# Kernel tuning notes

Measured on AMD Instinct MI355X. Metric: run time of the kernel, lower is better.

Reference implementation:

```python
import jax, jax.numpy as jnp
import numpy as np

N_NODES = 28


def _gcn_norm(edge_index, n):
    """PyG GCNConv normalization: add self-loops, sym-normalize by deg^-1/2."""
    loops = jnp.arange(n, dtype=edge_index.dtype)
    src = jnp.concatenate([edge_index[0], loops])
    dst = jnp.concatenate([edge_index[1], loops])
    ones = jnp.ones(src.shape[0], dtype=jnp.float32)
    deg = jax.ops.segment_sum(ones, dst, num_segments=n)  # in-degree incl. self-loop
    dinv = jnp.where(deg > 0, 1.0 / jnp.sqrt(deg), 0.0)
    norm = dinv[src] * dinv[dst]  # [E+N]
    return src, dst, norm


def _gcn_conv(x, W, b, src, dst, norm, n):
    # x: [B, N, Cin] -> [B, N, Cout]; linear first, then normalized scatter-add.
    h = jnp.einsum('bni,io->bno', x, W)
    msg = h[:, src, :] * norm[None, :, None]          # gather + edge scaling
    out = jnp.zeros_like(h).at[:, dst, :].add(msg)     # scatter-add over dst
    return out + b


def setup_inputs() -> dict:
    key = jax.random.key(0)
    k1, k2, k3, k4 = jax.random.split(key, 4)
    B, N, E, H = 65536, N_NODES, 756, 64
    x = jax.random.normal(k1, (B, N), dtype=jnp.float32)
    edge_index = jax.random.randint(k2, (2, E), 0, N, dtype=jnp.int64)
    W1 = jax.random.normal(k3, (1, H), dtype=jnp.float32) * (1.0 / np.sqrt(1.0))
    b1 = jnp.zeros((H,), dtype=jnp.float32)
    W2 = jax.random.normal(k4, (H, 1), dtype=jnp.float32) * (1.0 / np.sqrt(H))
    b2 = jnp.zeros((1,), dtype=jnp.float32)
    return {"x": x, "edge_index": edge_index, "W1": W1, "b1": b1, "W2": W2, "b2": b2}


def reference(x, edge_index, W1, b1, W2, b2):
    n = x.shape[1]
    src, dst, norm = _gcn_norm(edge_index, n)
    h = x[:, :, None]                                  # [B, N, 1] node features
    h = jax.nn.relu(_gcn_conv(h, W1, b1, src, dst, norm, n))
    # dropout(0.2) is identity in eval mode
    h = _gcn_conv(h, W2, b2, src, dst, norm, n)        # [B, N, 1]
    return h[:, :, 0]
```

## Files before the change

### kernel.cpp

```cpp
#include <hip/hip_runtime.h>
#include <math.h>

#define NN 28
#define NH 64

__global__ __launch_bounds__(256) void build_graph_kernel(
    const int* __restrict__ ei, int E,
    const float* __restrict__ W1, const float* __restrict__ b1,
    const float* __restrict__ W2, float* __restrict__ ws) {
  __shared__ float dinv[NN];
  __shared__ float A[NN * NN];
  __shared__ float cpos, cneg;
  __shared__ int flag;
  const int t = threadIdx.x;

  if (t < NN) dinv[t] = 1.0f;
  for (int i = t; i < NN * NN; i += blockDim.x) A[i] = 0.0f;
  if (t == 0) { cpos = 0.0f; cneg = 0.0f; flag = 0; }
  __syncthreads();

  for (int e = t; e < E; e += blockDim.x) {
    int d = ei[E + e];
    atomicAdd(&dinv[d], 1.0f);
  }
  __syncthreads();
  if (t < NN) dinv[t] = 1.0f / sqrtf(dinv[t]);
  __syncthreads();

  for (int e = t; e < E; e += blockDim.x) {
    int s = ei[e];
    int d = ei[E + e];
    atomicAdd(&A[d * NN + s], dinv[s] * dinv[d]);
  }
  if (t < NN) atomicAdd(&A[t * NN + t], dinv[t] * dinv[t]);

  if (t < NH) {
    float w1 = W1[t], w2 = W2[t];
    if (w1 > 0.0f)      atomicAdd(&cpos, w1 * w2);
    else if (w1 < 0.0f) atomicAdd(&cneg, w1 * w2);
    if (b1[t] != 0.0f) atomicOr(&flag, 1);
  }
  __syncthreads();

  for (int i = t; i < NN * NN; i += blockDim.x) ws[i] = A[i];
  if (t == 0) {
    ws[NN * NN]     = cpos;
    ws[NN * NN + 1] = cneg;
    ws[NN * NN + 2] = (float)flag;
  }
}

__global__ __launch_bounds__(256) void gcn_fwd_kernel(
    const float* __restrict__ x, const float* __restrict__ ws,
    const float* __restrict__ W1, const float* __restrict__ b1,
    const float* __restrict__ W2, const float* __restrict__ b2,
    float* __restrict__ out, int B) {
  const int b = blockIdx.x * blockDim.x + threadIdx.x;
  if (b >= B) return;

  const float4* xp = (const float4*)(x + (size_t)b * NN);
  float xv[NN];
#pragma unroll
  for (int k = 0; k < 7; ++k) {
    float4 v = xp[k];
    xv[4 * k + 0] = v.x; xv[4 * k + 1] = v.y;
    xv[4 * k + 2] = v.z; xv[4 * k + 3] = v.w;
  }

  float s[NN];
#pragma unroll
  for (int n = 0; n < NN; ++n) {
    float acc = 0.0f;
#pragma unroll
    for (int m = 0; m < NN; ++m) acc = fmaf(ws[n * NN + m], xv[m], acc);
    s[n] = acc;
  }

  const float cpos = ws[NN * NN];
  const float cneg = ws[NN * NN + 1];
  const bool  fast = (ws[NN * NN + 2] == 0.0f);

  float z[NN];
  if (fast) {
#pragma unroll
    for (int n = 0; n < NN; ++n)
      z[n] = s[n] * (s[n] > 0.0f ? cpos : cneg);
  } else {
#pragma unroll
    for (int n = 0; n < NN; ++n) z[n] = 0.0f;
    for (int o = 0; o < NH; ++o) {
      float w1 = W1[o], bb = b1[o], w2 = W2[o];
#pragma unroll
      for (int n = 0; n < NN; ++n)
        z[n] = fmaf(fmaxf(fmaf(s[n], w1, bb), 0.0f), w2, z[n]);
    }
  }

  const float bias2 = b2[0];
  float ov[NN];
#pragma unroll
  for (int n = 0; n < NN; ++n) {
    float acc = bias2;
#pragma unroll
    for (int m = 0; m < NN; ++m) acc = fmaf(ws[n * NN + m], z[m], acc);
    ov[n] = acc;
  }

  float4* op = (float4*)(out + (size_t)b * NN);
#pragma unroll
  for (int k = 0; k < 7; ++k) {
    float4 v;
    v.x = ov[4 * k + 0]; v.y = ov[4 * k + 1];
    v.z = ov[4 * k + 2]; v.w = ov[4 * k + 3];
    op[k] = v;
  }
}

extern "C" void kernel_launch(void* const* d_in, const int* in_sizes, int n_in,
                              void* d_out, int out_size, void* d_ws, size_t ws_size,
                              hipStream_t stream) {
  const float* x  = (const float*)d_in[0];
  const int*   ei = (const int*)d_in[1];
  const float* W1 = (const float*)d_in[2];
  const float* b1 = (const float*)d_in[3];
  const float* W2 = (const float*)d_in[4];
  const float* b2 = (const float*)d_in[5];
  float* out = (float*)d_out;
  float* ws  = (float*)d_ws;

  const int E = in_sizes[1] / 2;
  const int B = in_sizes[0] / NN;

  build_graph_kernel<<<1, 256, 0, stream>>>(ei, E, W1, b1, W2, ws);

  const int threads = 256;
  const int blocks = (B + threads - 1) / threads;
  gcn_fwd_kernel<<<blocks, threads, 0, stream>>>(x, ws, W1, b1, W2, b2, out, B);
}
```

Baseline: 87.97 us.

## Fuse graph build into forward kernel, rebuilding the adjacency in each block

Removes the separate single-block graph-building launch. Every block of the forward kernel now rebuilds the normalized 28x28 adjacency and the cpos/cneg constants in shared memory, then reads them as float4 from LDS instead of from global workspace. This drops one launch and the serial dependency between the two kernels. In exchange, every block (256 of them) redundantly reads 756 edges and does shared atomics plus extra barriers before its main work.

```diff
diff --git a/kernel.cpp b/kernel.cpp
--- a/kernel.cpp
+++ b/kernel.cpp
@@ -4,30 +4,28 @@
 #define NN 28
 #define NH 64
 
-__global__ __launch_bounds__(256) void build_graph_kernel(
-    const int* __restrict__ ei, int E,
+__global__ __launch_bounds__(256) void gcn_fused_kernel(
+    const float* __restrict__ x, const int* __restrict__ ei, int E,
     const float* __restrict__ W1, const float* __restrict__ b1,
-    const float* __restrict__ W2, float* __restrict__ ws) {
+    const float* __restrict__ W2, const float* __restrict__ b2,
+    float* __restrict__ out, int B) {
+  __shared__ __align__(16) float A[NN * NN];
   __shared__ float dinv[NN];
-  __shared__ float A[NN * NN];
-  __shared__ float cpos, cneg;
-  __shared__ int flag;
+  __shared__ float cpos_s, cneg_s;
+  __shared__ int flag_s;
   const int t = threadIdx.x;
 
   if (t < NN) dinv[t] = 1.0f;
-  for (int i = t; i < NN * NN; i += blockDim.x) A[i] = 0.0f;
-  if (t == 0) { cpos = 0.0f; cneg = 0.0f; flag = 0; }
+  for (int i = t; i < NN * NN; i += 256) A[i] = 0.0f;
+  if (t == 0) { cpos_s = 0.0f; cneg_s = 0.0f; flag_s = 0; }
   __syncthreads();
 
-  for (int e = t; e < E; e += blockDim.x) {
-    int d = ei[E + e];
-    atomicAdd(&dinv[d], 1.0f);
-  }
+  for (int e = t; e < E; e += 256) atomicAdd(&dinv[ei[E + e]], 1.0f);
   __syncthreads();
   if (t < NN) dinv[t] = 1.0f / sqrtf(dinv[t]);
   __syncthreads();
 
-  for (int e = t; e < E; e += blockDim.x) {
+  for (int e = t; e < E; e += 256) {
     int s = ei[e];
     int d = ei[E + e];
     atomicAdd(&A[d * NN + s], dinv[s] * dinv[d]);
@@ -36,26 +34,13 @@
 
   if (t < NH) {
     float w1 = W1[t], w2 = W2[t];
-    if (w1 > 0.0f)      atomicAdd(&cpos, w1 * w2);
-    else if (w1 < 0.0f) atomicAdd(&cneg, w1 * w2);
-    if (b1[t] != 0.0f) atomicOr(&flag, 1);
+    if (w1 > 0.0f)      atomicAdd(&cpos_s, w1 * w2);
+    else if (w1 < 0.0f) atomicAdd(&cneg_s, w1 * w2);
+    if (b1[t] != 0.0f) atomicOr(&flag_s, 1);
   }
   __syncthreads();
 
-  for (int i = t; i < NN * NN; i += blockDim.x) ws[i] = A[i];
-  if (t == 0) {
-    ws[NN * NN]     = cpos;
-    ws[NN * NN + 1] = cneg;
-    ws[NN * NN + 2] = (float)flag;
-  }
-}
-
-__global__ __launch_bounds__(256) void gcn_fwd_kernel(
-    const float* __restrict__ x, const float* __restrict__ ws,
-    const float* __restrict__ W1, const float* __restrict__ b1,
-    const float* __restrict__ W2, const float* __restrict__ b2,
-    float* __restrict__ out, int B) {
-  const int b = blockIdx.x * blockDim.x + threadIdx.x;
+  const int b = blockIdx.x * 256 + t;
   if (b >= B) return;
 
   const float4* xp = (const float4*)(x + (size_t)b * NN);
@@ -67,18 +52,26 @@
     xv[4 * k + 2] = v.z; xv[4 * k + 3] = v.w;
   }
 
+  const float4* A4 = (const float4*)A;
+
   float s[NN];
 #pragma unroll
   for (int n = 0; n < NN; ++n) {
     float acc = 0.0f;
 #pragma unroll
-    for (int m = 0; m < NN; ++m) acc = fmaf(ws[n * NN + m], xv[m], acc);
+    for (int k = 0; k < 7; ++k) {
+      float4 a = A4[n * 7 + k];
+      acc = fmaf(a.x, xv[4 * k + 0], acc);
+      acc = fmaf(a.y, xv[4 * k + 1], acc);
+      acc = fmaf(a.z, xv[4 * k + 2], acc);
+      acc = fmaf(a.w, xv[4 * k + 3], acc);
+    }
     s[n] = acc;
   }
 
-  const float cpos = ws[NN * NN];
-  const float cneg = ws[NN * NN + 1];
-  const bool  fast = (ws[NN * NN + 2] == 0.0f);
+  const float cpos = cpos_s;
+  const float cneg = cneg_s;
+  const bool  fast = (flag_s == 0);
 
   float z[NN];
   if (fast) {
@@ -102,7 +95,13 @@
   for (int n = 0; n < NN; ++n) {
     float acc = bias2;
 #pragma unroll
-    for (int m = 0; m < NN; ++m) acc = fmaf(ws[n * NN + m], z[m], acc);
+    for (int k = 0; k < 7; ++k) {
+      float4 a = A4[n * 7 + k];
+      acc = fmaf(a.x, z[4 * k + 0], acc);
+      acc = fmaf(a.y, z[4 * k + 1], acc);
+      acc = fmaf(a.z, z[4 * k + 2], acc);
+      acc = fmaf(a.w, z[4 * k + 3], acc);
+    }
     ov[n] = acc;
   }
 
@@ -126,14 +125,12 @@
   const float* W2 = (const float*)d_in[4];
   const float* b2 = (const float*)d_in[5];
   float* out = (float*)d_out;
-  float* ws  = (float*)d_ws;
 
   const int E = in_sizes[1] / 2;
   const int B = in_sizes[0] / NN;
 
-  build_graph_kernel<<<1, 256, 0, stream>>>(ei, E, W1, b1, W2, ws);
-
   const int threads = 256;
   const int blocks = (B + threads - 1) / threads;
-  gcn_fwd_kernel<<<blocks, threads, 0, stream>>>(x, ws, W1, b1, W2, b2, out, B);
+  gcn_fused_kernel<<<blocks, threads, 0, stream>>>(x, ei, E, W1, b1, W2, b2,
+                                                   out, B);
 }
```

After: 83.14 us. -5.5%, faster.
